# Kernel optimization log

Hardware: AMD Instinct MI355X
Metric: run time of the kernel (lower is better)

## Reference

```python
import jax, jax.numpy as jnp
import numpy as np

B, S, D_IN, D_MODEL, H = 4, 2048, 1024, 1024, 16
HD = D_MODEL // H  # head_dim = 64


def setup_inputs() -> dict:
    key = jax.random.key(0)
    ks = jax.random.split(key, 9)
    scale = 1.0 / np.sqrt(D_IN)
    return {
        "Q": jax.random.normal(ks[0], (B, S, D_IN), jnp.float32),
        "V": jax.random.normal(ks[1], (B, S, D_IN), jnp.float32),
        "K": jax.random.normal(ks[2], (B, S, D_IN), jnp.float32),
        "wq": jax.random.uniform(ks[3], (D_IN, D_MODEL), jnp.float32, -scale, scale),
        "bq": jax.random.uniform(ks[4], (D_MODEL,), jnp.float32, -scale, scale),
        "wk": jax.random.uniform(ks[5], (D_IN, D_MODEL), jnp.float32, -scale, scale),
        "bk": jax.random.uniform(ks[6], (D_MODEL,), jnp.float32, -scale, scale),
        "wv": jax.random.uniform(ks[7], (D_IN, D_MODEL), jnp.float32, -scale, scale),
        "bv": jax.random.uniform(ks[8], (D_MODEL,), jnp.float32, -scale, scale),
    }


def _split_heads(x):
    # [B,S,D] -> [B,H,S,HD]
    return x.reshape(B, S, H, HD).transpose(0, 2, 1, 3)


def reference(Q, V, K, wq, bq, wk, bk, wv, bv):
    q = _split_heads(Q @ wq + bq)
    k = _split_heads(K @ wk + bk)
    v = _split_heads(V @ wv + bv)
    scores = jnp.einsum("bhqd,bhkd->bhqk", q, k) / jnp.sqrt(jnp.float32(HD))
    weights = jax.nn.softmax(scores, axis=-1)
    out = jnp.einsum("bhqk,bhkd->bhqd", weights, v)
    return out.transpose(0, 2, 1, 3).reshape(B, S, D_MODEL)
```

## Files before the change

kernel.cpp:

```cpp
#include <hip/hip_runtime.h>

typedef unsigned short u16;
typedef __attribute__((ext_vector_type(8))) short bf16x8;
typedef __attribute__((ext_vector_type(4))) float f32x4;
typedef __attribute__((ext_vector_type(4))) unsigned short u16x4;
typedef __attribute__((ext_vector_type(2))) unsigned u32x2;

#define NB 4
#define NS 2048
#define DIN 1024
#define DM 1024
#define NH 16
#define HD 64
#define LOG2E 1.44269504f

__device__ __forceinline__ u16 f2bf(float f) {
  union { float f; unsigned u; } x; x.f = f;
  unsigned r = x.u + 0x7fffu + ((x.u >> 16) & 1u);
  return (u16)(r >> 16);
}

__device__ __forceinline__ void gl_lds16(const u16* g, u16* l) {
  __builtin_amdgcn_global_load_lds((const __attribute__((address_space(1))) void*)g,
                                   (__attribute__((address_space(3))) void*)l, 16, 0, 0);
}

__global__ void cvt_kernel(const float* __restrict__ Qp, const float* __restrict__ Kp,
                           const float* __restrict__ Vp, u16* __restrict__ oq,
                           u16* __restrict__ ok, u16* __restrict__ ov, int n4) {
  const float* s = blockIdx.y == 0 ? Qp : blockIdx.y == 1 ? Kp : Vp;
  u16* d = blockIdx.y == 0 ? oq : blockIdx.y == 1 ? ok : ov;
  int stride = gridDim.x * blockDim.x;
  for (int i = blockIdx.x * blockDim.x + threadIdx.x; i < n4; i += stride) {
    f32x4 v = ((const f32x4*)s)[i];
    u16x4 o = { f2bf(v.x), f2bf(v.y), f2bf(v.z), f2bf(v.w) };
    ((u16x4*)d)[i] = o;
  }
}

__global__ void wtrans_kernel(const float* __restrict__ wqp, const float* __restrict__ wkp,
                              const float* __restrict__ wvp, u16* __restrict__ oq,
                              u16* __restrict__ ok, u16* __restrict__ ov) {
  const float* W = blockIdx.z == 0 ? wqp : blockIdx.z == 1 ? wkp : wvp;
  u16* Wt = blockIdx.z == 0 ? oq : blockIdx.z == 1 ? ok : ov;
  __shared__ float tile[64][65];
  int n0 = blockIdx.x * 64, k0 = blockIdx.y * 64;
  int t = threadIdx.x;
#pragma unroll
  for (int i = 0; i < 16; i++) {
    int idx = t + i * 256;
    int r = idx >> 6, c = idx & 63;
    tile[r][c] = W[(size_t)(k0 + r) * DM + n0 + c];
  }
  __syncthreads();
#pragma unroll
  for (int i = 0; i < 16; i++) {
    int idx = t + i * 256;
    int r = idx >> 6, c = idx & 63;
    Wt[(size_t)(n0 + r) * DIN + k0 + c] = f2bf(tile[c][r]);
  }
}

__global__ __launch_bounds__(256) void proj_kernel(
    const u16* __restrict__ Xq, const u16* __restrict__ Xk, const u16* __restrict__ Xv,
    const u16* __restrict__ Wtq, const u16* __restrict__ Wtk, const u16* __restrict__ Wtv,
    const float* __restrict__ bq, const float* __restrict__ bk, const float* __restrict__ bv,
    u16* __restrict__ oq, u16* __restrict__ ok, u16* __restrict__ ov) {
  __shared__ __align__(16) u16 Abuf[128 * 64];
  __shared__ __align__(16) u16 Bbuf[128 * 64];
  const int z = blockIdx.z;
  const u16* X  = z == 0 ? Xq : z == 1 ? Xk : Xv;
  const u16* Wt = z == 0 ? Wtq : z == 1 ? Wtk : Wtv;
  const float* bias = z == 0 ? bq : z == 1 ? bk : bv;
  u16* out = z == 0 ? oq : z == 1 ? ok : ov;
  const int m0 = blockIdx.y * 128, n0 = blockIdx.x * 128;
  const int t = threadIdx.x, lane = t & 63, w = t >> 6;
  const int c = lane & 15, g = lane >> 4;
  const int wm = (w >> 1) * 64, wn = (w & 1) * 64;
  f32x4 acc[4][4] = {};
  for (int k0 = 0; k0 < DIN; k0 += 64) {
#pragma unroll
    for (int i = 0; i < 4; i++) {
      int idx = (w * 4 + i) * 64 + lane;
      int row = idx >> 3;
      int srck = (idx & 7) ^ (row & 7);
      gl_lds16(&X [(size_t)(m0 + row) * DIN + k0 + srck * 8], &Abuf[(w * 4 + i) * 512]);
      gl_lds16(&Wt[(size_t)(n0 + row) * DIN + k0 + srck * 8], &Bbuf[(w * 4 + i) * 512]);
    }
    __syncthreads();
#pragma unroll
    for (int ks = 0; ks < 2; ks++) {
      bf16x8 xf[4], wf[4];
      int chn = ((ks * 4 + g) ^ (c & 7)) * 8;
#pragma unroll
      for (int a = 0; a < 4; a++) {
        xf[a] = *(const bf16x8*)&Abuf[(wm + a * 16 + c) * 64 + chn];
        wf[a] = *(const bf16x8*)&Bbuf[(wn + a * 16 + c) * 64 + chn];
      }
      if (z < 2) {
#pragma unroll
        for (int i = 0; i < 4; i++)
#pragma unroll
          for (int j = 0; j < 4; j++)
            acc[i][j] = __builtin_amdgcn_mfma_f32_16x16x32_bf16(wf[i], xf[j], acc[i][j], 0, 0, 0);
      } else {
#pragma unroll
        for (int i = 0; i < 4; i++)
#pragma unroll
          for (int j = 0; j < 4; j++)
            acc[i][j] = __builtin_amdgcn_mfma_f32_16x16x32_bf16(xf[i], wf[j], acc[i][j], 0, 0, 0);
      }
    }
    __syncthreads();
  }
  if (z < 2) {
    const float sc = (z == 0) ? 0.125f : 1.0f;
#pragma unroll
    for (int i = 0; i < 4; i++) {
      int nb = n0 + wn + i * 16 + g * 4;
      int h = nb >> 6, d0 = nb & 63;
      f32x4 bv4 = *(const f32x4*)&bias[nb];
#pragma unroll
      for (int j = 0; j < 4; j++) {
        int mm = m0 + wm + j * 16 + c;
        int b = mm >> 11, s = mm & 2047;
        u16x4 pk;
#pragma unroll
        for (int r = 0; r < 4; r++) pk[r] = f2bf((acc[i][j][r] + bv4[r]) * sc);
        *(u16x4*)&out[((size_t)(b * NH + h) * NS + s) * HD + d0] = pk;
      }
    }
  } else {
#pragma unroll
    for (int j = 0; j < 4; j++) {
      int n = n0 + wn + j * 16 + c;
      int h = n >> 6, d = n & 63;
      float bvs = bias[n];
#pragma unroll
      for (int i = 0; i < 4; i++) {
        int mb = m0 + wm + i * 16 + g * 4;
        int b = mb >> 11, s0 = mb & 2047;
        u16x4 pk;
#pragma unroll
        for (int r = 0; r < 4; r++) pk[r] = f2bf(acc[i][j][r] + bvs);
        *(u16x4*)&out[((size_t)(b * NH + h) * HD + d) * NS + s0] = pk;
      }
    }
  }
}

__global__ __launch_bounds__(256, 2) void attn_kernel(
    const u16* __restrict__ q, const u16* __restrict__ k, const u16* __restrict__ vT,
    float* __restrict__ out) {
  __shared__ __align__(16) u16 kt[64 * 64];
  __shared__ __align__(16) u16 vt[64 * 64];
  __shared__ __align__(16) u16 pt_all[4][64 * 64];
  const int bh = blockIdx.y;
  const int t = threadIdx.x, lane = t & 63, w = t >> 6;
  const int c = lane & 15, g = lane >> 4;
  const int q0 = blockIdx.x * 256 + w * 64;
  u16* pt = pt_all[w];
  const u16* qsrc = q + ((size_t)bh * NS + q0) * HD;
  const u16* ksrc = k + (size_t)bh * NS * HD;
  const u16* vsrc = vT + (size_t)bh * HD * NS;
  const int srow = lane >> 3;
  const int skc = (lane & 7) ^ srow;
  bf16x8 qf[4][2];
#pragma unroll
  for (int grp = 0; grp < 4; grp++)
#pragma unroll
    for (int ks = 0; ks < 2; ks++)
      qf[grp][ks] = *(const bf16x8*)&qsrc[(grp * 16 + c) * HD + ks * 32 + g * 8];
  f32x4 o[4][4] = {};
  float lrun[4] = { 0.f, 0.f, 0.f, 0.f };
  for (int kt0 = 0; kt0 < NS; kt0 += 64) {
#pragma unroll
    for (int j = 0; j < 2; j++) {
      int row = w * 16 + j * 8 + srow;
      gl_lds16(&ksrc[(size_t)(kt0 + row) * HD + skc * 8], &kt[(w * 16 + j * 8) * 64]);
      gl_lds16(&vsrc[(size_t)row * NS + kt0 + skc * 8], &vt[(w * 16 + j * 8) * 64]);
    }
    __syncthreads();
    bf16x8 kf[4][2], vf[4][2];
#pragma unroll
    for (int kg = 0; kg < 4; kg++)
#pragma unroll
      for (int ks = 0; ks < 2; ks++) {
        kf[kg][ks] = *(const bf16x8*)&kt[(kg * 16 + c) * 64 + (((ks * 4 + g) ^ (c & 7)) * 8)];
        vf[kg][ks] = *(const bf16x8*)&vt[(kg * 16 + c) * 64 + (((ks * 4 + g) ^ (c & 7)) * 8)];
      }
#pragma unroll
    for (int grp = 0; grp < 4; grp++) {
      f32x4 s4[4] = {};
#pragma unroll
      for (int ks = 0; ks < 2; ks++)
#pragma unroll
        for (int kg = 0; kg < 4; kg++)
          s4[kg] = __builtin_amdgcn_mfma_f32_16x16x32_bf16(kf[kg][ks], qf[grp][ks], s4[kg], 0, 0, 0);
      float ls = 0.f;
#pragma unroll
      for (int kg = 0; kg < 4; kg++) {
        unsigned pu[4];
#pragma unroll
        for (int r = 0; r < 4; r++) {
          float p = exp2f(s4[kg][r] * LOG2E);
          ls += p;
          pu[r] = __float_as_uint(p) + 0x8000u;
        }
        u32x2 pk;
        pk.x = __builtin_amdgcn_perm(pu[1], pu[0], 0x07060302u);
        pk.y = __builtin_amdgcn_perm(pu[3], pu[2], 0x07060302u);
        *(u32x2*)&pt[(grp * 16 + c) * 64 + (((kg * 2 + (g >> 1)) ^ (c & 7)) * 8) + (g & 1) * 4] = pk;
      }
      lrun[grp] += ls;
    }
#pragma unroll
    for (int grp = 0; grp < 4; grp++) {
      bf16x8 pf[2];
#pragma unroll
      for (int ks = 0; ks < 2; ks++)
        pf[ks] = *(const bf16x8*)&pt[(grp * 16 + c) * 64 + (((ks * 4 + g) ^ (c & 7)) * 8)];
#pragma unroll
      for (int ks = 0; ks < 2; ks++)
#pragma unroll
        for (int dj = 0; dj < 4; dj++)
          o[grp][dj] = __builtin_amdgcn_mfma_f32_16x16x32_bf16(vf[dj][ks], pf[ks], o[grp][dj], 0, 0, 0);
    }
    __syncthreads();
  }
  const int b = bh >> 4, h = bh & 15;
#pragma unroll
  for (int grp = 0; grp < 4; grp++) {
    float l = lrun[grp];
    l += __shfl_xor(l, 16);
    l += __shfl_xor(l, 32);
    float inv = 1.f / l;
    int s = q0 + grp * 16 + c;
#pragma unroll
    for (int dj = 0; dj < 4; dj++) {
      f32x4 ov = o[grp][dj] * inv;
      *(f32x4*)&out[((size_t)b * NS + s) * DM + h * HD + dj * 16 + g * 4] = ov;
    }
  }
}

extern "C" void kernel_launch(void* const* d_in, const int* in_sizes, int n_in,
                              void* d_out, int out_size, void* d_ws, size_t ws_size,
                              hipStream_t stream) {
  const float* Q  = (const float*)d_in[0];
  const float* V  = (const float*)d_in[1];
  const float* K  = (const float*)d_in[2];
  const float* wq = (const float*)d_in[3];
  const float* bq = (const float*)d_in[4];
  const float* wk = (const float*)d_in[5];
  const float* bk = (const float*)d_in[6];
  const float* wv = (const float*)d_in[7];
  const float* bv = (const float*)d_in[8];
  float* out = (float*)d_out;
  char* ws = (char*)d_ws;
  const size_t NX = (size_t)NB * NS * DIN;
  const size_t XB = NX * 2;
  const size_t WB = (size_t)DIN * DM * 2;
  u16* Xq   = (u16*)(ws);
  u16* Xk   = (u16*)(ws + XB);
  u16* Xv   = (u16*)(ws + 2 * XB);
  u16* Wtq  = (u16*)(ws + 3 * XB);
  u16* Wtk  = (u16*)(ws + 3 * XB + WB);
  u16* Wtv  = (u16*)(ws + 3 * XB + 2 * WB);
  u16* qws  = (u16*)(ws + 3 * XB + 3 * WB);
  u16* kws  = (u16*)(ws + 4 * XB + 3 * WB);
  u16* vTws = (u16*)(ws + 5 * XB + 3 * WB);
  const int n4 = (int)(NX / 4);
  cvt_kernel<<<dim3(1024, 3), 256, 0, stream>>>(Q, K, V, Xq, Xk, Xv, n4);
  wtrans_kernel<<<dim3(16, 16, 3), 256, 0, stream>>>(wq, wk, wv, Wtq, Wtk, Wtv);
  proj_kernel<<<dim3(8, 64, 3), 256, 0, stream>>>(Xq, Xk, Xv, Wtq, Wtk, Wtv,
                                                  bq, bk, bv, qws, kws, vTws);
  attn_kernel<<<dim3(8, 64), 256, 0, stream>>>(qws, kws, vTws, out);
}
```

Baseline: 349.5 us.

## Fold log2e into Q scale, sum probabilities via MFMA, remap blocks for XCD locality

The softmax scale now includes log2e when Q is projected, so the attention loop calls exp2f directly without a multiply. The per-lane row-sum accumulation and the cross-lane shuffles at the end are replaced by an extra MFMA against a ones vector, which sums the bf16 probabilities that are also used for P·V. Both kernels switch to a 1-D grid with a swizzled block index. Consecutive blocks, which likely land on different XCDs, then share a head or weight tile, aiming for better L2 reuse. The trade-offs are extra MFMA work per tile and row sums taken from bf16-rounded values.

```diff
diff --git a/kernel.cpp b/kernel.cpp
--- a/kernel.cpp
+++ b/kernel.cpp
@@ -1,4 +1,5 @@
 #include <hip/hip_runtime.h>
+#include <hip/hip_bf16.h>
 
 typedef unsigned short u16;
 typedef __attribute__((ext_vector_type(8))) short bf16x8;
@@ -18,6 +19,12 @@
   union { float f; unsigned u; } x; x.f = f;
   unsigned r = x.u + 0x7fffu + ((x.u >> 16) & 1u);
   return (u16)(r >> 16);
+}
+
+__device__ __forceinline__ unsigned pk_bf16(float a, float b) {
+  union { __hip_bfloat162 h; unsigned u; } cv;
+  cv.h = __float22bfloat162_rn(make_float2(a, b));
+  return cv.u;
 }
 
 __device__ __forceinline__ void gl_lds16(const u16* g, u16* l) {
@@ -68,12 +75,16 @@
     u16* __restrict__ oq, u16* __restrict__ ok, u16* __restrict__ ov) {
   __shared__ __align__(16) u16 Abuf[128 * 64];
   __shared__ __align__(16) u16 Bbuf[128 * 64];
-  const int z = blockIdx.z;
+  const int bid = blockIdx.x;
+  const int xr = bid & 7;
+  const int nt = (bid >> 3) & 7;
+  const int mt = (bid >> 6) & 7;
+  const int z  = bid >> 9;
+  const int m0 = (mt * 8 + xr) * 128, n0 = nt * 128;
   const u16* X  = z == 0 ? Xq : z == 1 ? Xk : Xv;
   const u16* Wt = z == 0 ? Wtq : z == 1 ? Wtk : Wtv;
   const float* bias = z == 0 ? bq : z == 1 ? bk : bv;
   u16* out = z == 0 ? oq : z == 1 ? ok : ov;
-  const int m0 = blockIdx.y * 128, n0 = blockIdx.x * 128;
   const int t = threadIdx.x, lane = t & 63, w = t >> 6;
   const int c = lane & 15, g = lane >> 4;
   const int wm = (w >> 1) * 64, wn = (w & 1) * 64;
@@ -114,7 +125,7 @@
     __syncthreads();
   }
   if (z < 2) {
-    const float sc = (z == 0) ? 0.125f : 1.0f;
+    const float sc = (z == 0) ? 0.125f * LOG2E : 1.0f;
 #pragma unroll
     for (int i = 0; i < 4; i++) {
       int nb = n0 + wn + i * 16 + g * 4;
@@ -155,10 +166,14 @@
   __shared__ __align__(16) u16 kt[64 * 64];
   __shared__ __align__(16) u16 vt[64 * 64];
   __shared__ __align__(16) u16 pt_all[4][64 * 64];
-  const int bh = blockIdx.y;
+  const int bid = blockIdx.x;
+  const int xr = bid & 7;
+  const int qc = (bid >> 3) & 7;
+  const int h8 = bid >> 6;
+  const int bh = xr + 8 * h8;
   const int t = threadIdx.x, lane = t & 63, w = t >> 6;
   const int c = lane & 15, g = lane >> 4;
-  const int q0 = blockIdx.x * 256 + w * 64;
+  const int q0 = qc * 256 + w * 64;
   u16* pt = pt_all[w];
   const u16* qsrc = q + ((size_t)bh * NS + q0) * HD;
   const u16* ksrc = k + (size_t)bh * NS * HD;
@@ -171,8 +186,11 @@
 #pragma unroll
     for (int ks = 0; ks < 2; ks++)
       qf[grp][ks] = *(const bf16x8*)&qsrc[(grp * 16 + c) * HD + ks * 32 + g * 8];
+  bf16x8 ones;
+#pragma unroll
+  for (int i = 0; i < 8; i++) ones[i] = (short)0x3F80;
   f32x4 o[4][4] = {};
-  float lrun[4] = { 0.f, 0.f, 0.f, 0.f };
+  f32x4 ol[4] = {};
   for (int kt0 = 0; kt0 < NS; kt0 += 64) {
 #pragma unroll
     for (int j = 0; j < 2; j++) {
@@ -197,22 +215,13 @@
 #pragma unroll
         for (int kg = 0; kg < 4; kg++)
           s4[kg] = __builtin_amdgcn_mfma_f32_16x16x32_bf16(kf[kg][ks], qf[grp][ks], s4[kg], 0, 0, 0);
-      float ls = 0.f;
 #pragma unroll
       for (int kg = 0; kg < 4; kg++) {
-        unsigned pu[4];
-#pragma unroll
-        for (int r = 0; r < 4; r++) {
-          float p = exp2f(s4[kg][r] * LOG2E);
-          ls += p;
-          pu[r] = __float_as_uint(p) + 0x8000u;
-        }
         u32x2 pk;
-        pk.x = __builtin_amdgcn_perm(pu[1], pu[0], 0x07060302u);
-        pk.y = __builtin_amdgcn_perm(pu[3], pu[2], 0x07060302u);
+        pk.x = pk_bf16(exp2f(s4[kg][0]), exp2f(s4[kg][1]));
+        pk.y = pk_bf16(exp2f(s4[kg][2]), exp2f(s4[kg][3]));
         *(u32x2*)&pt[(grp * 16 + c) * 64 + (((kg * 2 + (g >> 1)) ^ (c & 7)) * 8) + (g & 1) * 4] = pk;
       }
-      lrun[grp] += ls;
     }
 #pragma unroll
     for (int grp = 0; grp < 4; grp++) {
@@ -221,20 +230,19 @@
       for (int ks = 0; ks < 2; ks++)
         pf[ks] = *(const bf16x8*)&pt[(grp * 16 + c) * 64 + (((ks * 4 + g) ^ (c & 7)) * 8)];
 #pragma unroll
-      for (int ks = 0; ks < 2; ks++)
+      for (int ks = 0; ks < 2; ks++) {
 #pragma unroll
         for (int dj = 0; dj < 4; dj++)
           o[grp][dj] = __builtin_amdgcn_mfma_f32_16x16x32_bf16(vf[dj][ks], pf[ks], o[grp][dj], 0, 0, 0);
+        ol[grp] = __builtin_amdgcn_mfma_f32_16x16x32_bf16(ones, pf[ks], ol[grp], 0, 0, 0);
+      }
     }
     __syncthreads();
   }
   const int b = bh >> 4, h = bh & 15;
 #pragma unroll
   for (int grp = 0; grp < 4; grp++) {
-    float l = lrun[grp];
-    l += __shfl_xor(l, 16);
-    l += __shfl_xor(l, 32);
-    float inv = 1.f / l;
+    float inv = 1.f / ol[grp][0];
     int s = q0 + grp * 16 + c;
 #pragma unroll
     for (int dj = 0; dj < 4; dj++) {
@@ -273,7 +281,7 @@
   const int n4 = (int)(NX / 4);
   cvt_kernel<<<dim3(1024, 3), 256, 0, stream>>>(Q, K, V, Xq, Xk, Xv, n4);
   wtrans_kernel<<<dim3(16, 16, 3), 256, 0, stream>>>(wq, wk, wv, Wtq, Wtk, Wtv);
-  proj_kernel<<<dim3(8, 64, 3), 256, 0, stream>>>(Xq, Xk, Xv, Wtq, Wtk, Wtv,
-                                                  bq, bk, bv, qws, kws, vTws);
-  attn_kernel<<<dim3(8, 64), 256, 0, stream>>>(qws, kws, vTws, out);
-}
+  proj_kernel<<<1536, 256, 0, stream>>>(Xq, Xk, Xv, Wtq, Wtk, Wtv,
+                                        bq, bk, bv, qws, kws, vTws);
+  attn_kernel<<<512, 256, 0, stream>>>(qws, kws, vTws, out);
+}
```

New measurement: 344.0 us. No clear change (-1.6%).
